# Optimization experiments

Hardware: AMD Instinct MI355X
Metric: run time of the kernel (lower is better)

## Reference

```python
import jax, jax.numpy as jnp
import numpy as np

B, IN, E, H, V, MAX_LEN = 512, 64, 512, 1024, 1024, 32
LN_EPS = 1e-5


def setup_inputs() -> dict:
    key = jax.random.key(0)
    ks = jax.random.split(key, 16)
    s = 0.02
    n = lambda k, shp: jax.random.normal(k, shp, jnp.float32) * s
    return {
        "x": jax.random.normal(ks[0], (B, IN), jnp.float32),
        "w_in": n(ks[1], (E, IN)), "b_in": jnp.zeros((E,), jnp.float32),
        "w_ih0": n(ks[2], (4 * H, E)), "w_hh0": n(ks[3], (4 * H, H)),
        "b_ih0": jnp.zeros((4 * H,), jnp.float32), "b_hh0": jnp.zeros((4 * H,), jnp.float32),
        "w_ih1": n(ks[4], (4 * H, H)), "w_hh1": n(ks[5], (4 * H, H)),
        "b_ih1": jnp.zeros((4 * H,), jnp.float32), "b_hh1": jnp.zeros((4 * H,), jnp.float32),
        "ln_g": jnp.ones((H,), jnp.float32), "ln_b": jnp.zeros((H,), jnp.float32),
        "w_out": n(ks[6], (V, H)), "b_out": jnp.zeros((V,), jnp.float32),
        "emb": n(ks[7], (V, E)),
    }


def _lstm_cell(x, h, c, w_ih, w_hh, b_ih, b_hh):
    # PyTorch LSTMCell: gates ordered (input, forget, cell, output)
    gates = x @ w_ih.T + h @ w_hh.T + b_ih + b_hh  # [B, 4H]
    i, f, g, o = jnp.split(gates, 4, axis=1)
    i, f, o = jax.nn.sigmoid(i), jax.nn.sigmoid(f), jax.nn.sigmoid(o)
    g = jnp.tanh(g)
    c2 = f * c + i * g
    h2 = o * jnp.tanh(c2)
    return h2, c2


def reference(x, w_in, b_in, w_ih0, w_hh0, b_ih0, b_hh0,
              w_ih1, w_hh1, b_ih1, b_hh1, ln_g, ln_b, w_out, b_out, emb):
    bsz = x.shape[0]
    hid = w_hh0.shape[1]
    inp = x @ w_in.T + b_in  # [B, E]
    z = jnp.zeros((bsz, hid), jnp.float32)
    init = (z, z, z, z, inp)

    def step(carry, _):
        h0, c0, h1, c1, cur = carry
        h0, c0 = _lstm_cell(cur, h0, c0, w_ih0, w_hh0, b_ih0, b_hh0)
        h1, c1 = _lstm_cell(h0, h1, c1, w_ih1, w_hh1, b_ih1, b_hh1)
        mu = jnp.mean(h1, axis=-1, keepdims=True)
        var = jnp.mean((h1 - mu) ** 2, axis=-1, keepdims=True)
        hn = (h1 - mu) / jnp.sqrt(var + LN_EPS) * ln_g + ln_b
        lp = jax.nn.log_softmax(hn @ w_out.T + b_out, axis=-1)  # [B, V]
        ent = -jnp.sum(jnp.exp(lp) * lp, axis=-1)  # [B]
        sym = jnp.argmax(lp, axis=-1)  # eval-mode (deterministic) path
        logprob = jnp.take_along_axis(lp, sym[:, None], axis=1)[:, 0]
        nxt = emb[sym]  # [B, E]
        return (h0, c0, h1, c1, nxt), (sym, logprob, ent)

    _, (seq, logits, ent) = jax.lax.scan(step, init, None, length=MAX_LEN)
    seq, logits, ent = seq.T, logits.T, ent.T  # [B, MAX_LEN]
    zcol_f = jnp.zeros((bsz, 1), jnp.float32)
    zcol_i = jnp.zeros((bsz, 1), seq.dtype)
    seq = jnp.concatenate([seq, zcol_i], axis=1)
    logits = jnp.concatenate([logits, zcol_f], axis=1)
    ent = jnp.concatenate([ent, zcol_f], axis=1)
    return seq, logits, ent
```

## Files before the change

### kernel.cpp

```cpp
#include <hip/hip_runtime.h>
#include <hip/hip_bf16.h>
#include <math.h>

#define BQ   512
#define EDIM 512
#define HDIM 1024
#define VDIM 1024
#define TLEN 32
#define TOUT 33
#define PLS  (BQ * VDIM)

typedef _Float16 half8  __attribute__((ext_vector_type(8)));
typedef _Float16 half4v __attribute__((ext_vector_type(4)));
typedef float    f32x16 __attribute__((ext_vector_type(16)));

__device__ __forceinline__ size_t packoff(int r, int k, int K) {
    return (size_t)(r >> 5) * (size_t)(32 * K) + (size_t)(k >> 4) * 512
         + (size_t)((k >> 3) & 1) * 256 + (size_t)(r & 31) * 8 + (size_t)(k & 7);
}

__device__ _Float16 g_curh[BQ*EDIM], g_curl[BQ*EDIM];
__device__ _Float16 g_h0h[BQ*HDIM], g_h0l[BQ*HDIM];
__device__ _Float16 g_h1h[BQ*HDIM], g_h1l[BQ*HDIM];
__device__ _Float16 g_hnh[BQ*HDIM], g_hnl[BQ*HDIM];
__device__ float    g_c0[BQ*HDIM], g_c1[BQ*HDIM];

__device__ _Float16 g_wih0h[4*HDIM*EDIM], g_wih0l[4*HDIM*EDIM];
__device__ _Float16 g_whh0h[4*HDIM*HDIM], g_whh0l[4*HDIM*HDIM];
__device__ _Float16 g_wih1h[4*HDIM*HDIM], g_wih1l[4*HDIM*HDIM];
__device__ _Float16 g_whh1h[4*HDIM*HDIM], g_whh1l[4*HDIM*HDIM];
__device__ _Float16 g_wouth[VDIM*HDIM],   g_woutl[VDIM*HDIM];

__device__ float g_gates[BQ * 4 * HDIM];
__device__ float g_part_lg[4 * PLS];
__device__ float g_bsum0[4*HDIM], g_bsum1[4*HDIM];

__global__ void init_kernel(float* __restrict__ out,
                            const float* __restrict__ bi0, const float* __restrict__ bh0,
                            const float* __restrict__ bi1, const float* __restrict__ bh1) {
    int i = blockIdx.x * 256 + threadIdx.x;
    g_c0[i] = 0.f; g_c1[i] = 0.f;
    g_h0h[i] = (_Float16)0.f; g_h0l[i] = (_Float16)0.f;
    g_h1h[i] = (_Float16)0.f; g_h1l[i] = (_Float16)0.f;
    if (i < 4 * HDIM) {
        g_bsum0[i] = bi0[i] + bh0[i];
        g_bsum1[i] = bi1[i] + bh1[i];
    }
    if (i < 3 * BQ) {
        int which = i / BQ, b = i % BQ;
        out[(size_t)which * BQ * TOUT + (size_t)b * TOUT + (TOUT - 1)] = 0.f;
    }
}

__global__ void split_pack_kernel(const float* __restrict__ w, _Float16* __restrict__ hi,
                                  _Float16* __restrict__ lo, int klog, int nquads) {
    int q = blockIdx.x * 256 + threadIdx.x;
    if (q >= nquads) return;
    int e = q * 4;
    int r = e >> klog, k = e & ((1 << klog) - 1);
    float4 v = ((const float4*)w)[q];
    half4v h, l;
    h[0] = (_Float16)v.x; l[0] = (_Float16)((v.x - (float)h[0]) * 4096.f);
    h[1] = (_Float16)v.y; l[1] = (_Float16)((v.y - (float)h[1]) * 4096.f);
    h[2] = (_Float16)v.z; l[2] = (_Float16)((v.z - (float)h[2]) * 4096.f);
    h[3] = (_Float16)v.w; l[3] = (_Float16)((v.w - (float)h[3]) * 4096.f);
    size_t po = packoff(r, k, 1 << klog);
    *(half4v*)&hi[po] = h;
    *(half4v*)&lo[po] = l;
}

__device__ __forceinline__ void split1(float x, _Float16* hp, _Float16* lp) {
    _Float16 h = (_Float16)x;
    *hp = h;
    *lp = (_Float16)((x - (float)h) * 4096.f);
}

__global__ __launch_bounds__(256, 2) void gemm_nolds(
    const _Float16* __restrict__ Ah1, const _Float16* __restrict__ Al1, int K1,
    const _Float16* __restrict__ Wh1, const _Float16* __restrict__ Wl1,
    const _Float16* __restrict__ Ah2, const _Float16* __restrict__ Al2, int K2,
    const _Float16* __restrict__ Wh2, const _Float16* __restrict__ Wl2,
    const float* __restrict__ bias, float* __restrict__ outp,
    int N, int S, int P)
{
    int tid = threadIdx.x;
    int l = tid & 63, w = tid >> 6;
    int lr = l & 31, lq = l >> 5;
    int mh = w >> 1, nh = w & 1;

    int wb = blockIdx.x;
    int xcd = wb & 7, q = wb >> 3;
    int nb = xcd * P + (q % P);
    int rest = q / P;
    int s = rest % S;
    int mb = rest / S;

    int kch1 = K1 / S, kch2 = K2 / S;
    int n1 = kch1 >> 5;
    int nit = n1 + (kch2 >> 5);

    size_t aoff1 = (size_t)(mb*2+mh) * (size_t)(32*K1) + (size_t)((s*kch1) >> 4) * 512 + (size_t)l*8;
    size_t boff1 = (size_t)(nb*2+nh) * (size_t)(32*K1) + (size_t)((s*kch1) >> 4) * 512 + (size_t)l*8;
    const _Float16* pAh1 = Ah1 + aoff1;
    const _Float16* pAl1 = Al1 + aoff1;
    const _Float16* pWh1 = Wh1 + boff1;
    const _Float16* pWl1 = Wl1 + boff1;
    const _Float16 *pAh2 = pAh1, *pAl2 = pAl1, *pWh2 = pWh1, *pWl2 = pWl1;
    if (K2 > 0) {
        size_t aoff2 = (size_t)(mb*2+mh) * (size_t)(32*K2) + (size_t)((s*kch2) >> 4) * 512 + (size_t)l*8;
        size_t boff2 = (size_t)(nb*2+nh) * (size_t)(32*K2) + (size_t)((s*kch2) >> 4) * 512 + (size_t)l*8;
        pAh2 = Ah2 + aoff2; pAl2 = Al2 + aoff2;
        pWh2 = Wh2 + boff2; pWl2 = Wl2 + boff2;
    }

    f32x16 accM = {}, accL = {};

#define LOAD_IT(it, A, B) { \
        int it_ = (it); size_t off_; \
        const _Float16 *ah_, *al_, *wh_, *wl_; \
        if (it_ < n1) { off_ = (size_t)it_ * 1024;        ah_ = pAh1; al_ = pAl1; wh_ = pWh1; wl_ = pWl1; } \
        else          { off_ = (size_t)(it_ - n1) * 1024; ah_ = pAh2; al_ = pAl2; wh_ = pWh2; wl_ = pWl2; } \
        A[0][0] = *(const half8*)(ah_ + off_);       A[0][1] = *(const half8*)(ah_ + off_ + 512); \
        A[1][0] = *(const half8*)(al_ + off_);       A[1][1] = *(const half8*)(al_ + off_ + 512); \
        B[0][0] = *(const half8*)(wh_ + off_);       B[0][1] = *(const half8*)(wh_ + off_ + 512); \
        B[1][0] = *(const half8*)(wl_ + off_);       B[1][1] = *(const half8*)(wl_ + off_ + 512); \
    }

#define COMP_IT(A, B) { \
        _Pragma("unroll") \
        for (int kh_ = 0; kh_ < 2; ++kh_) { \
            accM = __builtin_amdgcn_mfma_f32_32x32x16_f16(A[0][kh_], B[0][kh_], accM, 0, 0, 0); \
            accL = __builtin_amdgcn_mfma_f32_32x32x16_f16(A[0][kh_], B[1][kh_], accL, 0, 0, 0); \
            accL = __builtin_amdgcn_mfma_f32_32x32x16_f16(A[1][kh_], B[0][kh_], accL, 0, 0, 0); \
        } \
    }

    half8 A0[2][2], B0[2][2], A1[2][2], B1[2][2];
    half8 A2[2][2], B2[2][2], A3[2][2], B3[2][2];
    LOAD_IT(0, A0, B0);
    LOAD_IT(1, A1, B1);
    for (int itp = 0; itp < nit; itp += 4) {
        if (itp + 2 < nit) LOAD_IT(itp + 2, A2, B2);
        COMP_IT(A0, B0);
        if (itp + 3 < nit) LOAD_IT(itp + 3, A3, B3);
        COMP_IT(A1, B1);
        if (itp + 4 < nit) LOAD_IT(itp + 4, A0, B0);
        COMP_IT(A2, B2);
        if (itp + 5 < nit) LOAD_IT(itp + 5, A1, B1);
        COMP_IT(A3, B3);
    }
#undef LOAD_IT
#undef COMP_IT

    int n = nb * 64 + nh * 32 + lr;
    int m0 = mb * 64 + mh * 32;
    float bv = bias ? bias[n] : 0.f;
    float* op = outp + (size_t)s * BQ * N;
    #pragma unroll
    for (int r = 0; r < 16; ++r) {
        int row = (r & 3) + 8 * (r >> 2) + 4 * lq;
        op[(size_t)(m0 + row) * N + n] = accM[r] + accL[r] * (1.f / 4096.f) + bv;
    }
}

#define GBK 16
#define GPAD 68
__global__ __launch_bounds__(256) void gemm_in(const float* __restrict__ x,
                                               const float* __restrict__ w_in,
                                               const float* __restrict__ b_in) {
    __shared__ __align__(16) float As[GBK][GPAD];
    __shared__ __align__(16) float Bs[GBK][GPAD];
    int tid = threadIdx.x;
    int tx = tid & 15, ty = tid >> 4;
    int m0 = blockIdx.y * 64, n0 = blockIdx.x * 64;
    int lm = tid >> 2, lk = (tid & 3) << 2;
    const int K = 64;
    float acc[4][4] = {};
    for (int k0 = 0; k0 < K; k0 += GBK) {
        float4 av = *(const float4*)(x + (size_t)(m0 + lm) * K + k0 + lk);
        float4 wv = *(const float4*)(w_in + (size_t)(n0 + lm) * K + k0 + lk);
        As[lk + 0][lm] = av.x; As[lk + 1][lm] = av.y;
        As[lk + 2][lm] = av.z; As[lk + 3][lm] = av.w;
        Bs[lk + 0][lm] = wv.x; Bs[lk + 1][lm] = wv.y;
        Bs[lk + 2][lm] = wv.z; Bs[lk + 3][lm] = wv.w;
        __syncthreads();
        #pragma unroll
        for (int kk = 0; kk < GBK; ++kk) {
            float4 a  = *(const float4*)&As[kk][ty * 4];
            float4 bq = *(const float4*)&Bs[kk][tx * 4];
            float aa[4] = {a.x, a.y, a.z, a.w};
            float bb[4] = {bq.x, bq.y, bq.z, bq.w};
            #pragma unroll
            for (int i = 0; i < 4; ++i)
                #pragma unroll
                for (int j = 0; j < 4; ++j)
                    acc[i][j] = fmaf(aa[i], bb[j], acc[i][j]);
        }
        __syncthreads();
    }
    #pragma unroll
    for (int i = 0; i < 4; ++i) {
        int m = m0 + ty * 4 + i;
        int n = n0 + tx * 4;
        half4v h, lo;
        #pragma unroll
        for (int j = 0; j < 4; ++j) {
            float v = acc[i][j] + b_in[n + j];
            _Float16 hv = (_Float16)v;
            h[j] = hv;
            lo[j] = (_Float16)((v - (float)hv) * 4096.f);
        }
        size_t po = packoff(m, n, EDIM);
        *(half4v*)&g_curh[po] = h;
        *(half4v*)&g_curl[po] = lo;
    }
}

__device__ __forceinline__ float sigm(float x) { return 1.f / (1.f + expf(-x)); }

__global__ void lstm0_kernel() {
    int qidx = blockIdx.x * 256 + threadIdx.x;
    int b = qidx >> 8;
    int j = (qidx & 255) * 4;
    size_t base = (size_t)b * 4096;
    float4 G[4];
    #pragma unroll
    for (int g = 0; g < 4; ++g) G[g] = *(const float4*)&g_gates[base + g * 1024 + j];
    size_t hb = (size_t)b * HDIM + j;
    float4 cin = *(const float4*)&g_c0[hb];
    float ci[4] = {cin.x, cin.y, cin.z, cin.w};
    float gi[4] = {G[0].x, G[0].y, G[0].z, G[0].w};
    float gf[4] = {G[1].x, G[1].y, G[1].z, G[1].w};
    float gg[4] = {G[2].x, G[2].y, G[2].z, G[2].w};
    float go[4] = {G[3].x, G[3].y, G[3].z, G[3].w};
    float c[4], h[4];
    half4v hh, hl;
    #pragma unroll
    for (int r = 0; r < 4; ++r) {
        c[r] = sigm(gf[r]) * ci[r] + sigm(gi[r]) * tanhf(gg[r]);
        h[r] = sigm(go[r]) * tanhf(c[r]);
        _Float16 hi16 = (_Float16)h[r];
        hh[r] = hi16;
        hl[r] = (_Float16)((h[r] - (float)hi16) * 4096.f);
    }
    *(float4*)&g_c0[hb] = {c[0], c[1], c[2], c[3]};
    size_t po = packoff(b, j, HDIM);
    *(half4v*)&g_h0h[po] = hh;
    *(half4v*)&g_h0l[po] = hl;
}

__global__ __launch_bounds__(256) void lstm1_ln_kernel(
    const float* __restrict__ ln_g, const float* __restrict__ ln_b)
{
    __shared__ float sbuf[4];
    int b = blockIdx.x, tid = threadIdx.x;
    int lane = tid & 63, wid = tid >> 6;
    int j = tid * 4;
    size_t base = (size_t)b * 4096;
    float4 G[4];
    #pragma unroll
    for (int g = 0; g < 4; ++g) G[g] = *(const float4*)&g_gates[base + g * 1024 + j];
    size_t hb = (size_t)b * HDIM + j;
    float4 cin = *(const float4*)&g_c1[hb];
    float ci[4] = {cin.x, cin.y, cin.z, cin.w};
    float gi[4] = {G[0].x, G[0].y, G[0].z, G[0].w};
    float gf[4] = {G[1].x, G[1].y, G[1].z, G[1].w};
    float gg[4] = {G[2].x, G[2].y, G[2].z, G[2].w};
    float go[4] = {G[3].x, G[3].y, G[3].z, G[3].w};
    float c[4], h[4];
    float sum = 0.f;
    #pragma unroll
    for (int r = 0; r < 4; ++r) {
        c[r] = sigm(gf[r]) * ci[r] + sigm(gi[r]) * tanhf(gg[r]);
        h[r] = sigm(go[r]) * tanhf(c[r]);
        sum += h[r];
    }
    *(float4*)&g_c1[hb] = {c[0], c[1], c[2], c[3]};
    size_t po = packoff(b, j, HDIM);
    half4v h1h, h1l;
    #pragma unroll
    for (int r = 0; r < 4; ++r) {
        _Float16 hi16 = (_Float16)h[r];
        h1h[r] = hi16;
        h1l[r] = (_Float16)((h[r] - (float)hi16) * 4096.f);
    }
    *(half4v*)&g_h1h[po] = h1h;
    *(half4v*)&g_h1l[po] = h1l;

    for (int off = 32; off > 0; off >>= 1) sum += __shfl_down(sum, off, 64);
    if (lane == 0) sbuf[wid] = sum;
    __syncthreads();
    float mu = (sbuf[0] + sbuf[1] + sbuf[2] + sbuf[3]) * (1.f / HDIM);
    __syncthreads();
    float sq = 0.f;
    #pragma unroll
    for (int r = 0; r < 4; ++r) { float d = h[r] - mu; sq += d * d; }
    for (int off = 32; off > 0; off >>= 1) sq += __shfl_down(sq, off, 64);
    if (lane == 0) sbuf[wid] = sq;
    __syncthreads();
    float var = (sbuf[0] + sbuf[1] + sbuf[2] + sbuf[3]) * (1.f / HDIM);
    float rstd = 1.f / sqrtf(var + 1e-5f);
    half4v nh, nl;
    #pragma unroll
    for (int r = 0; r < 4; ++r) {
        float hn = (h[r] - mu) * rstd * ln_g[j + r] + ln_b[j + r];
        _Float16 hi16 = (_Float16)hn;
        nh[r] = hi16;
        nl[r] = (_Float16)((hn - (float)hi16) * 4096.f);
    }
    *(half4v*)&g_hnh[po] = nh;
    *(half4v*)&g_hnl[po] = nl;
}

__global__ __launch_bounds__(256) void softmax_row_kernel(
    const float* __restrict__ b_out, const float* __restrict__ emb,
    float* __restrict__ out, int t)
{
    __shared__ float swv[4];
    __shared__ int   swi[4];
    __shared__ float sZ[4], sS[4];
    __shared__ float s_max;
    __shared__ int   s_idx;
    int b = blockIdx.x, tid = threadIdx.x;
    int lane = tid & 63, wid = tid >> 6;
    size_t base = (size_t)b * VDIM + 4 * tid;
    float4 xv = *(const float4*)&b_out[4 * tid];
    #pragma unroll
    for (int s = 0; s < 4; ++s) {
        float4 p = *(const float4*)&g_part_lg[(size_t)s * PLS + base];
        xv.x += p.x; xv.y += p.y; xv.z += p.z; xv.w += p.w;
    }

    float mv = xv.x; int mi = 4 * tid;
    if (xv.y > mv) { mv = xv.y; mi = 4 * tid + 1; }
    if (xv.z > mv) { mv = xv.z; mi = 4 * tid + 2; }
    if (xv.w > mv) { mv = xv.w; mi = 4 * tid + 3; }
    for (int off = 32; off > 0; off >>= 1) {
        float ov = __shfl_down(mv, off, 64);
        int   oi = __shfl_down(mi, off, 64);
        if (ov > mv || (ov == mv && oi < mi)) { mv = ov; mi = oi; }
    }
    if (lane == 0) { swv[wid] = mv; swi[wid] = mi; }
    __syncthreads();
    if (tid == 0) {
        mv = swv[0]; mi = swi[0];
        for (int w = 1; w < 4; ++w)
            if (swv[w] > mv || (swv[w] == mv && swi[w] < mi)) { mv = swv[w]; mi = swi[w]; }
        s_max = mv; s_idx = mi;
    }
    __syncthreads();
    float xmax = s_max;

    float sv[4] = {xv.x - xmax, xv.y - xmax, xv.z - xmax, xv.w - xmax};
    float z = 0.f, s1 = 0.f;
    #pragma unroll
    for (int r = 0; r < 4; ++r) { float e = expf(sv[r]); z += e; s1 += e * sv[r]; }
    for (int off = 32; off > 0; off >>= 1) {
        z  += __shfl_down(z, off, 64);
        s1 += __shfl_down(s1, off, 64);
    }
    if (lane == 0) { sZ[wid] = z; sS[wid] = s1; }
    __syncthreads();
    if (tid == 0) {
        float Z = sZ[0] + sZ[1] + sZ[2] + sZ[3];
        float S1 = sS[0] + sS[1] + sS[2] + sS[3];
        float logZ = logf(Z);
        float ent = logZ - S1 / Z;
        out[(size_t)b * TOUT + t]                         = (float)s_idx;
        out[(size_t)BQ * TOUT + (size_t)b * TOUT + t]     = -logZ;
        out[(size_t)2 * BQ * TOUT + (size_t)b * TOUT + t] = ent;
    }
    __syncthreads();
    int sym = s_idx;
    const float* e = emb + (size_t)sym * EDIM;
    for (int j = tid; j < EDIM; j += 256) {
        size_t po = packoff(b, j, EDIM);
        split1(e[j], &g_curh[po], &g_curl[po]);
    }
}

extern "C" void kernel_launch(void* const* d_in, const int* in_sizes, int n_in,
                              void* d_out, int out_size, void* d_ws, size_t ws_size,
                              hipStream_t stream) {
    const float* x     = (const float*)d_in[0];
    const float* w_in  = (const float*)d_in[1];
    const float* b_in  = (const float*)d_in[2];
    const float* w_ih0 = (const float*)d_in[3];
    const float* w_hh0 = (const float*)d_in[4];
    const float* b_ih0 = (const float*)d_in[5];
    const float* b_hh0 = (const float*)d_in[6];
    const float* w_ih1 = (const float*)d_in[7];
    const float* w_hh1 = (const float*)d_in[8];
    const float* b_ih1 = (const float*)d_in[9];
    const float* b_hh1 = (const float*)d_in[10];
    const float* ln_g  = (const float*)d_in[11];
    const float* ln_b  = (const float*)d_in[12];
    const float* w_out = (const float*)d_in[13];
    const float* b_out = (const float*)d_in[14];
    const float* emb   = (const float*)d_in[15];
    float* out = (float*)d_out;

    _Float16 *wih0h, *wih0l, *whh0h, *whh0l, *wih1h, *wih1l, *whh1h, *whh1l, *wouth, *woutl;
    hipGetSymbolAddress((void**)&wih0h, HIP_SYMBOL(g_wih0h));
    hipGetSymbolAddress((void**)&wih0l, HIP_SYMBOL(g_wih0l));
    hipGetSymbolAddress((void**)&whh0h, HIP_SYMBOL(g_whh0h));
    hipGetSymbolAddress((void**)&whh0l, HIP_SYMBOL(g_whh0l));
    hipGetSymbolAddress((void**)&wih1h, HIP_SYMBOL(g_wih1h));
    hipGetSymbolAddress((void**)&wih1l, HIP_SYMBOL(g_wih1l));
    hipGetSymbolAddress((void**)&whh1h, HIP_SYMBOL(g_whh1h));
    hipGetSymbolAddress((void**)&whh1l, HIP_SYMBOL(g_whh1l));
    hipGetSymbolAddress((void**)&wouth, HIP_SYMBOL(g_wouth));
    hipGetSymbolAddress((void**)&woutl, HIP_SYMBOL(g_woutl));
    _Float16 *curh, *curl, *h0h, *h0l, *h1h, *h1l, *hnh, *hnl;
    hipGetSymbolAddress((void**)&curh, HIP_SYMBOL(g_curh));
    hipGetSymbolAddress((void**)&curl, HIP_SYMBOL(g_curl));
    hipGetSymbolAddress((void**)&h0h, HIP_SYMBOL(g_h0h));
    hipGetSymbolAddress((void**)&h0l, HIP_SYMBOL(g_h0l));
    hipGetSymbolAddress((void**)&h1h, HIP_SYMBOL(g_h1h));
    hipGetSymbolAddress((void**)&h1l, HIP_SYMBOL(g_h1l));
    hipGetSymbolAddress((void**)&hnh, HIP_SYMBOL(g_hnh));
    hipGetSymbolAddress((void**)&hnl, HIP_SYMBOL(g_hnl));
    float *gates, *part_lg, *bsum0, *bsum1;
    hipGetSymbolAddress((void**)&gates, HIP_SYMBOL(g_gates));
    hipGetSymbolAddress((void**)&part_lg, HIP_SYMBOL(g_part_lg));
    hipGetSymbolAddress((void**)&bsum0, HIP_SYMBOL(g_bsum0));
    hipGetSymbolAddress((void**)&bsum1, HIP_SYMBOL(g_bsum1));

    init_kernel<<<(BQ * HDIM) / 256, 256, 0, stream>>>(out, b_ih0, b_hh0, b_ih1, b_hh1);

    split_pack_kernel<<<(4*HDIM*EDIM/4 + 255)/256, 256, 0, stream>>>(w_ih0, wih0h, wih0l, 9,  4*HDIM*EDIM/4);
    split_pack_kernel<<<(4*HDIM*HDIM/4 + 255)/256, 256, 0, stream>>>(w_hh0, whh0h, whh0l, 10, 4*HDIM*HDIM/4);
    split_pack_kernel<<<(4*HDIM*HDIM/4 + 255)/256, 256, 0, stream>>>(w_ih1, wih1h, wih1l, 10, 4*HDIM*HDIM/4);
    split_pack_kernel<<<(4*HDIM*HDIM/4 + 255)/256, 256, 0, stream>>>(w_hh1, whh1h, whh1l, 10, 4*HDIM*HDIM/4);
    split_pack_kernel<<<(VDIM*HDIM/4 + 255)/256, 256, 0, stream>>>(w_out, wouth, woutl, 10, VDIM*HDIM/4);

    gemm_in<<<dim3(EDIM / 64, BQ / 64), 256, 0, stream>>>(x, w_in, b_in);

    for (int t = 0; t < TLEN; ++t) {
        gemm_nolds<<<512, 256, 0, stream>>>(
            curh, curl, EDIM, wih0h, wih0l,
            h0h, h0l, HDIM, whh0h, whh0l,
            bsum0, gates, 4 * HDIM, 1, 8);
        lstm0_kernel<<<(BQ * HDIM / 4) / 256, 256, 0, stream>>>();

        gemm_nolds<<<512, 256, 0, stream>>>(
            h0h, h0l, HDIM, wih1h, wih1l,
            h1h, h1l, HDIM, whh1h, whh1l,
            bsum1, gates, 4 * HDIM, 1, 8);
        lstm1_ln_kernel<<<BQ, 256, 0, stream>>>(ln_g, ln_b);

        gemm_nolds<<<512, 256, 0, stream>>>(
            hnh, hnl, HDIM, wouth, woutl,
            (const _Float16*)nullptr, (const _Float16*)nullptr, 0,
            (const _Float16*)nullptr, (const _Float16*)nullptr,
            (const float*)nullptr, part_lg, VDIM, 4, 2);

        softmax_row_kernel<<<BQ, 256, 0, stream>>>(b_out, emb, out, t);
    }
}
```

Baseline: 3.234 ms.

## Share activation tiles through LDS with async global_load_lds pipeline in GEMM

Replaces the register-only GEMM with a version whose block tile is 64x128. The activation hi/lo tiles are loaded once per block into a 4-slot LDS ring using global_load_lds and shared by all four waves, while each wave streams its own weight tiles into registers. Each wave now computes two 32x32 output tiles, so activation reuse doubles and the grid halves. In exchange it adds per-iteration barriers, hand-tuned vmcnt waits and fewer blocks, which lowers occupancy and latency hiding.

Result: faster. 3.127 ms (-3.3%).

```diff
diff --git a/kernel.cpp b/kernel.cpp
--- a/kernel.cpp
+++ b/kernel.cpp
@@ -13,6 +13,10 @@
 typedef _Float16 half8  __attribute__((ext_vector_type(8)));
 typedef _Float16 half4v __attribute__((ext_vector_type(4)));
 typedef float    f32x16 __attribute__((ext_vector_type(16)));
+
+#define GLOAD_LDS16(gp, lp) __builtin_amdgcn_global_load_lds( \
+    (const __attribute__((address_space(1))) void*)(gp),      \
+    (__attribute__((address_space(3))) void*)(lp), 16, 0, 0)
 
 __device__ __forceinline__ size_t packoff(int r, int k, int K) {
     return (size_t)(r >> 5) * (size_t)(32 * K) + (size_t)(k >> 4) * 512
@@ -75,91 +79,122 @@
     *lp = (_Float16)((x - (float)h) * 4096.f);
 }
 
-__global__ __launch_bounds__(256, 2) void gemm_nolds(
+__global__ __launch_bounds__(256) void gemm_pipe(
     const _Float16* __restrict__ Ah1, const _Float16* __restrict__ Al1, int K1,
     const _Float16* __restrict__ Wh1, const _Float16* __restrict__ Wl1,
     const _Float16* __restrict__ Ah2, const _Float16* __restrict__ Al2, int K2,
     const _Float16* __restrict__ Wh2, const _Float16* __restrict__ Wl2,
     const float* __restrict__ bias, float* __restrict__ outp,
-    int N, int S, int P)
+    int N, int S, int NTP)
 {
+    __shared__ __align__(16) _Float16 sA[4][2][2][2][512];
     int tid = threadIdx.x;
     int l = tid & 63, w = tid >> 6;
     int lr = l & 31, lq = l >> 5;
-    int mh = w >> 1, nh = w & 1;
+    int plw = w >> 1, mhw = w & 1;
 
     int wb = blockIdx.x;
     int xcd = wb & 7, q = wb >> 3;
-    int nb = xcd * P + (q % P);
-    int rest = q / P;
+    int nt = xcd * NTP + q % NTP;
+    int rest = q / NTP;
     int s = rest % S;
     int mb = rest / S;
 
-    int kch1 = K1 / S, kch2 = K2 / S;
+    int kch1 = K1 / S, kch2 = (K2 > 0) ? (K2 / S) : 0;
     int n1 = kch1 >> 5;
     int nit = n1 + (kch2 >> 5);
 
-    size_t aoff1 = (size_t)(mb*2+mh) * (size_t)(32*K1) + (size_t)((s*kch1) >> 4) * 512 + (size_t)l*8;
-    size_t boff1 = (size_t)(nb*2+nh) * (size_t)(32*K1) + (size_t)((s*kch1) >> 4) * 512 + (size_t)l*8;
-    const _Float16* pAh1 = Ah1 + aoff1;
-    const _Float16* pAl1 = Al1 + aoff1;
-    const _Float16* pWh1 = Wh1 + boff1;
-    const _Float16* pWl1 = Wl1 + boff1;
-    const _Float16 *pAh2 = pAh1, *pAl2 = pAl1, *pWh2 = pWh1, *pWl2 = pWl1;
+    const _Float16* pA1 = (plw ? Al1 : Ah1)
+        + (size_t)(mb*2 + mhw) * (size_t)(32*K1) + (size_t)((s*kch1) >> 4) * 512 + (size_t)l*8;
+    const _Float16* pWh1 = Wh1
+        + (size_t)(nt*4 + w) * (size_t)(32*K1) + (size_t)((s*kch1) >> 4) * 512 + (size_t)l*8;
+    const _Float16* pWl1 = Wl1
+        + (size_t)(nt*4 + w) * (size_t)(32*K1) + (size_t)((s*kch1) >> 4) * 512 + (size_t)l*8;
+    const _Float16 *pA2 = pA1, *pWh2 = pWh1, *pWl2 = pWl1;
     if (K2 > 0) {
-        size_t aoff2 = (size_t)(mb*2+mh) * (size_t)(32*K2) + (size_t)((s*kch2) >> 4) * 512 + (size_t)l*8;
-        size_t boff2 = (size_t)(nb*2+nh) * (size_t)(32*K2) + (size_t)((s*kch2) >> 4) * 512 + (size_t)l*8;
-        pAh2 = Ah2 + aoff2; pAl2 = Al2 + aoff2;
-        pWh2 = Wh2 + boff2; pWl2 = Wl2 + boff2;
-    }
-
-    f32x16 accM = {}, accL = {};
-
-#define LOAD_IT(it, A, B) { \
-        int it_ = (it); size_t off_; \
-        const _Float16 *ah_, *al_, *wh_, *wl_; \
-        if (it_ < n1) { off_ = (size_t)it_ * 1024;        ah_ = pAh1; al_ = pAl1; wh_ = pWh1; wl_ = pWl1; } \
-        else          { off_ = (size_t)(it_ - n1) * 1024; ah_ = pAh2; al_ = pAl2; wh_ = pWh2; wl_ = pWl2; } \
-        A[0][0] = *(const half8*)(ah_ + off_);       A[0][1] = *(const half8*)(ah_ + off_ + 512); \
-        A[1][0] = *(const half8*)(al_ + off_);       A[1][1] = *(const half8*)(al_ + off_ + 512); \
-        B[0][0] = *(const half8*)(wh_ + off_);       B[0][1] = *(const half8*)(wh_ + off_ + 512); \
-        B[1][0] = *(const half8*)(wl_ + off_);       B[1][1] = *(const half8*)(wl_ + off_ + 512); \
-    }
-
-#define COMP_IT(A, B) { \
-        _Pragma("unroll") \
-        for (int kh_ = 0; kh_ < 2; ++kh_) { \
-            accM = __builtin_amdgcn_mfma_f32_32x32x16_f16(A[0][kh_], B[0][kh_], accM, 0, 0, 0); \
-            accL = __builtin_amdgcn_mfma_f32_32x32x16_f16(A[0][kh_], B[1][kh_], accL, 0, 0, 0); \
-            accL = __builtin_amdgcn_mfma_f32_32x32x16_f16(A[1][kh_], B[0][kh_], accL, 0, 0, 0); \
-        } \
-    }
-
-    half8 A0[2][2], B0[2][2], A1[2][2], B1[2][2];
-    half8 A2[2][2], B2[2][2], A3[2][2], B3[2][2];
-    LOAD_IT(0, A0, B0);
-    LOAD_IT(1, A1, B1);
-    for (int itp = 0; itp < nit; itp += 4) {
-        if (itp + 2 < nit) LOAD_IT(itp + 2, A2, B2);
-        COMP_IT(A0, B0);
-        if (itp + 3 < nit) LOAD_IT(itp + 3, A3, B3);
-        COMP_IT(A1, B1);
-        if (itp + 4 < nit) LOAD_IT(itp + 4, A0, B0);
-        COMP_IT(A2, B2);
-        if (itp + 5 < nit) LOAD_IT(itp + 5, A1, B1);
-        COMP_IT(A3, B3);
-    }
-#undef LOAD_IT
-#undef COMP_IT
-
-    int n = nb * 64 + nh * 32 + lr;
-    int m0 = mb * 64 + mh * 32;
+        pA2 = (plw ? Al2 : Ah2)
+            + (size_t)(mb*2 + mhw) * (size_t)(32*K2) + (size_t)((s*kch2) >> 4) * 512 + (size_t)l*8;
+        pWh2 = Wh2
+            + (size_t)(nt*4 + w) * (size_t)(32*K2) + (size_t)((s*kch2) >> 4) * 512 + (size_t)l*8;
+        pWl2 = Wl2
+            + (size_t)(nt*4 + w) * (size_t)(32*K2) + (size_t)((s*kch2) >> 4) * 512 + (size_t)l*8;
+    }
+
+    f32x16 accM0 = {}, accM1 = {}, accL0 = {}, accL1 = {};
+    half8 B0h[2], B0l[2], B1h[2], B1l[2], B2h[2], B2l[2], B3h[2], B3l[2];
+
+#define STAGE(IT, SLOT, BH, BL)                                                \
+    {                                                                          \
+        int it_ = (IT);                                                        \
+        bool g1_ = it_ < n1;                                                   \
+        const _Float16* ap_ = g1_ ? pA1 : pA2;                                 \
+        const _Float16* wh_ = g1_ ? pWh1 : pWh2;                               \
+        const _Float16* wl_ = g1_ ? pWl1 : pWl2;                               \
+        size_t off_ = (size_t)(g1_ ? it_ : it_ - n1) * 1024;                   \
+        GLOAD_LDS16(ap_ + off_,       &sA[SLOT][plw][mhw][0][0]);              \
+        GLOAD_LDS16(ap_ + off_ + 512, &sA[SLOT][plw][mhw][1][0]);              \
+        BH[0] = *(const half8*)(wh_ + off_);                                   \
+        BH[1] = *(const half8*)(wh_ + off_ + 512);                             \
+        BL[0] = *(const half8*)(wl_ + off_);                                   \
+        BL[1] = *(const half8*)(wl_ + off_ + 512);                             \
+    }
+
+#define COMPUTE(BUF, BH, BL)                                                   \
+    {                                                                          \
+        _Pragma("unroll")                                                      \
+        for (int kh_ = 0; kh_ < 2; ++kh_) {                                    \
+            half8 ah0 = *(const half8*)&sA[BUF][0][0][kh_][(size_t)l * 8];     \
+            half8 ah1 = *(const half8*)&sA[BUF][0][1][kh_][(size_t)l * 8];     \
+            half8 al0 = *(const half8*)&sA[BUF][1][0][kh_][(size_t)l * 8];     \
+            half8 al1 = *(const half8*)&sA[BUF][1][1][kh_][(size_t)l * 8];     \
+            accM0 = __builtin_amdgcn_mfma_f32_32x32x16_f16(ah0, BH[kh_], accM0, 0, 0, 0); \
+            accM1 = __builtin_amdgcn_mfma_f32_32x32x16_f16(ah1, BH[kh_], accM1, 0, 0, 0); \
+            accL0 = __builtin_amdgcn_mfma_f32_32x32x16_f16(ah0, BL[kh_], accL0, 0, 0, 0); \
+            accL1 = __builtin_amdgcn_mfma_f32_32x32x16_f16(ah1, BL[kh_], accL1, 0, 0, 0); \
+            accL0 = __builtin_amdgcn_mfma_f32_32x32x16_f16(al0, BH[kh_], accL0, 0, 0, 0); \
+            accL1 = __builtin_amdgcn_mfma_f32_32x32x16_f16(al1, BH[kh_], accL1, 0, 0, 0); \
+        }                                                                      \
+    }
+
+#define WAITSYNC(IT)                                                           \
+    {                                                                          \
+        if ((IT) < nit - 2)      asm volatile("s_waitcnt vmcnt(12)" ::: "memory"); \
+        else if ((IT) == nit - 2) asm volatile("s_waitcnt vmcnt(6)"  ::: "memory"); \
+        else                      asm volatile("s_waitcnt vmcnt(0)"  ::: "memory"); \
+        __builtin_amdgcn_sched_barrier(0);                                     \
+        __builtin_amdgcn_s_barrier();                                          \
+    }
+
+#define ITER(IT, BUF, BHc, BLc, BHn, BLn)                                      \
+    {                                                                          \
+        if ((IT) + 2 < nit) STAGE((IT) + 2, ((BUF) + 2) & 3, BHn, BLn);        \
+        WAITSYNC(IT);                                                          \
+        COMPUTE(BUF, BHc, BLc);                                                \
+    }
+
+    STAGE(0, 0, B0h, B0l);
+    STAGE(1, 1, B1h, B1l);
+
+    for (int base = 0; base < nit; base += 4) {
+        ITER(base + 0, 0, B0h, B0l, B2h, B2l);
+        ITER(base + 1, 1, B1h, B1l, B3h, B3l);
+        ITER(base + 2, 2, B2h, B2l, B0h, B0l);
+        ITER(base + 3, 3, B3h, B3l, B1h, B1l);
+    }
+#undef ITER
+#undef WAITSYNC
+#undef COMPUTE
+#undef STAGE
+
+    int n = nt * 128 + w * 32 + lr;
+    int m0 = mb * 64;
     float bv = bias ? bias[n] : 0.f;
     float* op = outp + (size_t)s * BQ * N;
     #pragma unroll
     for (int r = 0; r < 16; ++r) {
         int row = (r & 3) + 8 * (r >> 2) + 4 * lq;
-        op[(size_t)(m0 + row) * N + n] = accM[r] + accL[r] * (1.f / 4096.f) + bv;
+        op[(size_t)(m0 + row) * N + n]      = accM0[r] + accL0[r] * (1.f / 4096.f) + bv;
+        op[(size_t)(m0 + 32 + row) * N + n] = accM1[r] + accL1[r] * (1.f / 4096.f) + bv;
     }
 }
 
@@ -437,23 +472,23 @@
     gemm_in<<<dim3(EDIM / 64, BQ / 64), 256, 0, stream>>>(x, w_in, b_in);
 
     for (int t = 0; t < TLEN; ++t) {
-        gemm_nolds<<<512, 256, 0, stream>>>(
+        gemm_pipe<<<256, 256, 0, stream>>>(
             curh, curl, EDIM, wih0h, wih0l,
             h0h, h0l, HDIM, whh0h, whh0l,
-            bsum0, gates, 4 * HDIM, 1, 8);
+            bsum0, gates, 4 * HDIM, 1, 4);
         lstm0_kernel<<<(BQ * HDIM / 4) / 256, 256, 0, stream>>>();
 
-        gemm_nolds<<<512, 256, 0, stream>>>(
+        gemm_pipe<<<256, 256, 0, stream>>>(
             h0h, h0l, HDIM, wih1h, wih1l,
             h1h, h1l, HDIM, whh1h, whh1l,
-            bsum1, gates, 4 * HDIM, 1, 8);
+            bsum1, gates, 4 * HDIM, 1, 4);
         lstm1_ln_kernel<<<BQ, 256, 0, stream>>>(ln_g, ln_b);
 
-        gemm_nolds<<<512, 256, 0, stream>>>(
+        gemm_pipe<<<256, 256, 0, stream>>>(
             hnh, hnl, HDIM, wouth, woutl,
             (const _Float16*)nullptr, (const _Float16*)nullptr, 0,
             (const _Float16*)nullptr, (const _Float16*)nullptr,
-            (const float*)nullptr, part_lg, VDIM, 4, 2);
+            (const float*)nullptr, part_lg, VDIM, 4, 1);
 
         softmax_row_kernel<<<BQ, 256, 0, stream>>>(b_out, emb, out, t);
     }
```
